# Optimization experiments

Hardware: AMD Instinct MI355X
Metric: run time of the kernel (lower is better)

The kernel has to match this reference:

```python
import jax, jax.numpy as jnp
import numpy as np

N, E, D = 100000, 200000, 300
NUM_EDGE_EMB = [6, 3]
BN_EPS = 1e-5


def setup_inputs() -> dict:
    key = jax.random.key(0)
    ks = jax.random.split(key, 10)
    return {
        "node_feats": jax.random.normal(ks[0], (N, D), jnp.float32),
        "src": jax.random.randint(ks[1], (E,), 0, N),
        "dst": jax.random.randint(ks[2], (E,), 0, N),
        "edge_feat0": jax.random.randint(ks[3], (E,), 0, NUM_EDGE_EMB[0]),
        "edge_feat1": jax.random.randint(ks[4], (E,), 0, NUM_EDGE_EMB[1]),
        # edge 'MLP' with num_layers=1 == Linear(num_emb, D) on one-hot indices
        "emb_w0": jax.random.normal(ks[5], (NUM_EDGE_EMB[0], D), jnp.float32) * 0.1,
        "emb_b0": jnp.zeros((D,), jnp.float32),
        "emb_w1": jax.random.normal(ks[6], (NUM_EDGE_EMB[1], D), jnp.float32) * 0.1,
        "emb_b1": jnp.zeros((D,), jnp.float32),
        # GIN update MLP: Linear(D, 2D) -> ReLU -> Linear(2D, D)
        "mlp_w1": jax.random.normal(ks[7], (D, 2 * D), jnp.float32) * (1.0 / np.sqrt(D)),
        "mlp_b1": jnp.zeros((2 * D,), jnp.float32),
        "mlp_w2": jax.random.normal(ks[8], (2 * D, D), jnp.float32) * (1.0 / np.sqrt(2 * D)),
        "mlp_b2": jnp.zeros((D,), jnp.float32),
        "bn_gamma": jnp.ones((D,), jnp.float32),
        "bn_beta": jnp.zeros((D,), jnp.float32),
    }


def reference(node_feats, src, dst, edge_feat0, edge_feat1,
              emb_w0, emb_b0, emb_w1, emb_b1,
              mlp_w1, mlp_b1, mlp_w2, mlp_b2,
              bn_gamma, bn_beta):
    n = node_feats.shape[0]
    # sum of per-variable edge embeddings (one-hot linear == lookup + bias)
    edge_emb = (emb_w0[edge_feat0] + emb_b0) + (emb_w1[edge_feat1] + emb_b1)  # (E, D)
    # u_add_e message, sum-reduce onto destination nodes
    msgs = node_feats[src] + edge_emb                                         # (E, D)
    agg = jax.ops.segment_sum(msgs, dst, num_segments=n)                      # (N, D)
    # GIN update MLP
    h = jax.nn.relu(agg @ mlp_w1 + mlp_b1)
    h = h @ mlp_w2 + mlp_b2
    # BatchNorm1d (training-mode forward: biased batch stats)
    mean = jnp.mean(h, axis=0)
    var = jnp.var(h, axis=0)
    h = (h - mean) * jax.lax.rsqrt(var + BN_EPS) * bn_gamma + bn_beta
    return h
```

## Files before the change

### kernel.cpp

```cpp
#include <hip/hip_runtime.h>
#include <stdint.h>


typedef __attribute__((ext_vector_type(8))) short short8;
typedef __attribute__((ext_vector_type(4))) short short4v;
typedef __attribute__((ext_vector_type(4))) float float4v;

__device__ inline unsigned short f2b(float f) {
  union { float f; unsigned int i; } v; v.f = f;
  unsigned int i = v.i;
  i += 0x7fffu + ((i >> 16) & 1u);
  return (unsigned short)(i >> 16);
}

__device__ __forceinline__ void gl_lds16(const short* g, short* l) {
  __builtin_amdgcn_global_load_lds(
      (const __attribute__((address_space(1))) unsigned int*)g,
      (__attribute__((address_space(3))) unsigned int*)l,
      16, 0, 0);
}

__global__ void transpose_pad(const float* __restrict__ in, short* __restrict__ out,
                              int R, int C, int outStride, int total) {
  int idx = blockIdx.x * blockDim.x + threadIdx.x;
  if (idx >= total) return;
  int r = idx / C, c = idx - r * C;
  out[(size_t)c * outStride + r] = (short)f2b(in[idx]);
}

__global__ void build_w01(const float* __restrict__ w0, const float* __restrict__ w1,
                          float* __restrict__ w01, int D, int NUM1, int total) {
  int i = blockIdx.x * blockDim.x + threadIdx.x;
  if (i >= total) return;
  int f01 = i / D, d = i - f01 * D;
  int f0 = f01 / NUM1, f1 = f01 - f0 * NUM1;
  w01[i] = w0[f0 * D + d] + w1[f1 * D + d];
}

__global__ void count_deg(const int* __restrict__ dst, int* __restrict__ deg, int E) {
  int e = blockIdx.x * blockDim.x + threadIdx.x;
  if (e < E) atomicAdd(&deg[dst[e]], 1);
}

__global__ void scan1(const int* __restrict__ deg, int* __restrict__ offp,
                      int* __restrict__ bsum, int n) {
  __shared__ int sh[256];
  const int t = threadIdx.x;
  const int base = blockIdx.x * 1024 + t * 4;
  int v[4], s = 0;
#pragma unroll
  for (int j = 0; j < 4; ++j) { int i = base + j; v[j] = (i < n) ? deg[i] : 0; s += v[j]; }
  sh[t] = s;
  __syncthreads();
  for (int d = 1; d < 256; d <<= 1) {
    int x = (t >= d) ? sh[t - d] : 0;
    __syncthreads();
    sh[t] += x;
    __syncthreads();
  }
  int excl = (t > 0) ? sh[t - 1] : 0;
  if (t == 255) bsum[blockIdx.x] = sh[255];
#pragma unroll
  for (int j = 0; j < 4; ++j) { int i = base + j; if (i < n) offp[i] = excl; excl += v[j]; }
}

__global__ void scan2(int* __restrict__ bsum, int nb) {
  __shared__ int sh[256];
  const int t = threadIdx.x;
  sh[t] = (t < nb) ? bsum[t] : 0;
  __syncthreads();
  for (int d = 1; d < 256; d <<= 1) {
    int x = (t >= d) ? sh[t - d] : 0;
    __syncthreads();
    sh[t] += x;
    __syncthreads();
  }
  if (t < nb) bsum[t] = (t > 0) ? sh[t - 1] : 0;
}

__global__ void fill_csr(const int* __restrict__ dst, const int* __restrict__ src,
                         const int* __restrict__ ef0, const int* __restrict__ ef1,
                         const int* __restrict__ offp, const int* __restrict__ bsum,
                         int* __restrict__ tmp, int2* __restrict__ ebp, int NUM1, int E) {
  int e = blockIdx.x * blockDim.x + threadIdx.x;
  if (e >= E) return;
  int dn = dst[e];
  int pos = offp[dn] + bsum[dn >> 10] + atomicAdd(&tmp[dn], 1);
  ebp[pos] = make_int2(src[e], ef0[e] * NUM1 + ef1[e]);
}

__global__ void gather_agg(const float* __restrict__ nf, const float* __restrict__ w01,
                           const float* __restrict__ b0f, const float* __restrict__ b1f,
                           const int* __restrict__ deg, const int* __restrict__ offp,
                           const int* __restrict__ bsum, const int2* __restrict__ ebp,
                           unsigned short* __restrict__ aggb,
                           int D, int ldab, int total) {
  int idx = blockIdx.x * blockDim.x + threadIdx.x;
  if (idx >= total) return;
  const int quads = ldab >> 2;
  int node = idx / quads;
  int q = idx - node * quads;
  int d = q * 4;
  unsigned short* op = &aggb[(size_t)node * ldab + d];
  if (d >= D) {
    short4v z = {0, 0, 0, 0};
    *(short4v*)op = z;
    return;
  }
  int dg = deg[node];
  int o = offp[node] + bsum[node >> 10];
  float4v acc = {0.f, 0.f, 0.f, 0.f};
  for (int j = 0; j < dg; ++j) {
    int2 p = ebp[o + j];
    float4v nv = *(const float4v*)&nf[(size_t)p.x * D + d];
    float4v wv = *(const float4v*)&w01[(size_t)p.y * D + d];
    acc += nv + wv;
  }
  float4v bb = *(const float4v*)&b0f[d];
  float4v b2v = *(const float4v*)&b1f[d];
  acc += (float)dg * (bb + b2v);
  short4v r;
#pragma unroll
  for (int j = 0; j < 4; ++j) r[j] = (short)f2b(acc[j]);
  *(short4v*)op = r;
}

template<bool RELU, bool STATS, bool CF32>
__global__ __launch_bounds__(256, 6)
void gemm_lds(const short* __restrict__ A, int lda,
              const short* __restrict__ BT, int ldbt,
              const float* __restrict__ bias,
              void* __restrict__ Cv, int ldc, int storeN,
              int M, int Nn, int KP, int ncolb,
              float* __restrict__ colsum, float* __restrict__ colsumsq) {
  constexpr int BM = 128, BN = 64, BK = 32;
  __shared__ __align__(16) short Al[BM * BK];
  __shared__ __align__(16) short Bl[BN * BK];

  const int nwg = gridDim.x;
  const int b = blockIdx.x;
  const int qq = nwg >> 3, rr = nwg & 7;
  const int xcd = b & 7, ii = b >> 3;
  const int w = ((xcd < rr) ? xcd * (qq + 1) : rr * (qq + 1) + (xcd - rr) * qq) + ii;
  const int by = w / ncolb, bx = w - by * ncolb;
  const int m0 = by * BM, n0 = bx * BN;

  const int t = threadIdx.x;
  const int wave = t >> 6, lane = t & 63, quad = lane >> 4, lr = lane & 15;
  const int wm = (wave >> 1) * 64, wn = (wave & 1) * 32;

  const int au = lane & 3;
  const int arow0 = (wave * 2 + 0) * 16 + (lane >> 2);
  const int arow1 = (wave * 2 + 1) * 16 + (lane >> 2);
  const int asw0 = au ^ ((arow0 ^ (arow0 >> 2)) & 3);
  const int asw1 = au ^ ((arow1 ^ (arow1 >> 2)) & 3);
  const short* asrc0 = A + (size_t)(m0 + arow0) * lda + asw0 * 8;
  const short* asrc1 = A + (size_t)(m0 + arow1) * lda + asw1 * 8;
  short* adst0 = &Al[(wave * 2 + 0) * 512];
  short* adst1 = &Al[(wave * 2 + 1) * 512];
  const int brow = wave * 16 + (lane >> 2);
  const int bsw = au ^ ((brow ^ (brow >> 2)) & 3);
  const short* bsrc = BT + (size_t)(n0 + brow) * ldbt + bsw * 8;
  short* bdst = &Bl[wave * 512];

  int aoff[4], boff[2];
#pragma unroll
  for (int mi = 0; mi < 4; ++mi) {
    int r = wm + mi * 16 + lr;
    aoff[mi] = r * BK + (quad ^ ((r ^ (r >> 2)) & 3)) * 8;
  }
#pragma unroll
  for (int ni = 0; ni < 2; ++ni) {
    int r = wn + ni * 16 + lr;
    boff[ni] = r * BK + (quad ^ ((r ^ (r >> 2)) & 3)) * 8;
  }

  const float4v fzero = {0.f, 0.f, 0.f, 0.f};
  float4v acc[4][2];
#pragma unroll
  for (int mi = 0; mi < 4; ++mi) {
    acc[mi][0] = fzero; acc[mi][1] = fzero;
  }

  for (int k0 = 0; k0 < KP; k0 += BK) {
    __syncthreads();
    gl_lds16(asrc0 + k0, adst0);
    gl_lds16(asrc1 + k0, adst1);
    gl_lds16(bsrc + k0, bdst);
    __syncthreads();
    short8 af[4], bfr[2];
#pragma unroll
    for (int mi = 0; mi < 4; ++mi) af[mi] = *(const short8*)&Al[aoff[mi]];
#pragma unroll
    for (int ni = 0; ni < 2; ++ni) bfr[ni] = *(const short8*)&Bl[boff[ni]];
#pragma unroll
    for (int mi = 0; mi < 4; ++mi) {
      acc[mi][0] = __builtin_amdgcn_mfma_f32_16x16x32_bf16(af[mi], bfr[0], acc[mi][0], 0, 0, 0);
      acc[mi][1] = __builtin_amdgcn_mfma_f32_16x16x32_bf16(af[mi], bfr[1], acc[mi][1], 0, 0, 0);
    }
  }

#pragma unroll
  for (int ni = 0; ni < 2; ++ni) {
    int gn = n0 + wn + ni * 16 + lr;
    bool store_c = (gn < storeN);
    bool ncol = (gn < Nn);
    float bv = ncol ? bias[gn] : 0.f;
    float s = 0.f, q = 0.f;
#pragma unroll
    for (int mi = 0; mi < 4; ++mi) {
      int gmb = m0 + wm + mi * 16 + quad * 4;
#pragma unroll
      for (int r = 0; r < 4; ++r) {
        int gm = gmb + r;
        float v = acc[mi][ni][r] + bv;
        if (RELU) v = fmaxf(v, 0.f);
        if (gm < M && store_c) {
          if constexpr (CF32) ((float*)Cv)[(size_t)gm * ldc + gn] = v;
          else ((unsigned short*)Cv)[(size_t)gm * ldc + gn] = f2b(v);
          if (STATS && ncol) { s += v; q += v * v; }
        }
      }
    }
    if constexpr (STATS) {
      s += __shfl_xor(s, 16); q += __shfl_xor(q, 16);
      s += __shfl_xor(s, 32); q += __shfl_xor(q, 32);
      if (quad == 0 && ncol) {
        unsafeAtomicAdd(&colsum[gn], s);
        unsafeAtomicAdd(&colsumsq[gn], q);
      }
    }
  }
}

__global__ void bn_finalize(const float* __restrict__ colsum, const float* __restrict__ colsumsq,
                            const float* __restrict__ gamma, const float* __restrict__ beta,
                            float2* __restrict__ ss, int D, float invN) {
  int d = blockIdx.x * blockDim.x + threadIdx.x;
  if (d >= D) return;
  float mean = colsum[d] * invN;
  float var = fmaxf(colsumsq[d] * invN - mean * mean, 0.f);
  float sc = rsqrtf(var + 1e-5f) * gamma[d];
  float sh = beta[d] - mean * sc;
  ss[d] = make_float2(sc, sh);
}

__global__ void bn_apply4(float4v* __restrict__ out, const float2* __restrict__ ss,
                          int total4, int cquads) {
  int idx = blockIdx.x * blockDim.x + threadIdx.x;
  if (idx >= total4) return;
  int c = (idx % cquads) * 4;
  float4v v = out[idx];
  float2 p0 = ss[c], p1 = ss[c + 1], p2 = ss[c + 2], p3 = ss[c + 3];
  v[0] = v[0] * p0.x + p0.y;
  v[1] = v[1] * p1.x + p1.y;
  v[2] = v[2] * p2.x + p2.y;
  v[3] = v[3] * p3.x + p3.y;
  out[idx] = v;
}

__global__ void bn_apply1(float* __restrict__ out, const float2* __restrict__ ss,
                          int total, int D) {
  int idx = blockIdx.x * blockDim.x + threadIdx.x;
  if (idx >= total) return;
  float2 p = ss[idx % D];
  out[idx] = out[idx] * p.x + p.y;
}

extern "C" void kernel_launch(void* const* d_in, const int* in_sizes, int n_in,
                              void* d_out, int out_size, void* d_ws, size_t ws_size,
                              hipStream_t stream) {
  const float* nf  = (const float*)d_in[0];
  const int*   src = (const int*)d_in[1];
  const int*   dst = (const int*)d_in[2];
  const int*   ef0 = (const int*)d_in[3];
  const int*   ef1 = (const int*)d_in[4];
  const float* ew0 = (const float*)d_in[5];
  const float* eb0 = (const float*)d_in[6];
  const float* ew1 = (const float*)d_in[7];
  const float* eb1 = (const float*)d_in[8];
  const float* w1  = (const float*)d_in[9];
  const float* b1  = (const float*)d_in[10];
  const float* w2  = (const float*)d_in[11];
  const float* b2  = (const float*)d_in[12];
  const float* gam = (const float*)d_in[13];
  const float* bet = (const float*)d_in[14];

  const int D = in_sizes[13];
  const int N = in_sizes[0] / D;
  const int E = in_sizes[1];
  const int H = in_sizes[10];
  const int NUM0 = in_sizes[5] / D;
  const int NUM1 = in_sizes[7] / D;
  const int KP1 = (D + 31) / 32 * 32;
  const int KP2 = (H + 31) / 32 * 32;
  const int NCB1 = (H + 63) / 64;
  const int NCB2 = (D + 63) / 64;
  const int BROWS1 = NCB1 * 64;
  const int BROWS2 = NCB2 * 64;
  const int nrowb = (N + 127) / 128;
  const int MP = nrowb * 128;
  const int nb  = (N + 1023) / 1024;

  char* ws = (char*)d_ws;
  size_t off = 0;
  float* colsum   = (float*)(ws + off); off += 4096;
  float* colsumsq = (float*)(ws + off); off += 4096;
  short* wT1      = (short*)(ws + off); off += (size_t)BROWS1 * KP1 * 2;
  short* wT2      = (short*)(ws + off); off += (size_t)BROWS2 * KP2 * 2;
  int*   deg      = (int*)(ws + off);   off += (size_t)N * 4;
  int*   tmp      = (int*)(ws + off);   off += (size_t)N * 4;
  size_t zero_bytes = off;
  float2* ss      = (float2*)(ws + off); off += 4096;
  float* w01      = (float*)(ws + off);  off += (size_t)NUM0 * NUM1 * D * 4;
  int*   offp     = (int*)(ws + off);    off += (size_t)N * 4;
  int*   bsum     = (int*)(ws + off);    off += 4096;
  int2*  ebp      = (int2*)(ws + off);   off += (size_t)E * 8;
  unsigned short* aggb = (unsigned short*)(ws + off); off += (size_t)MP * KP1 * 2;
  short* h1       = (short*)(ws + off);  off += (size_t)MP * KP2 * 2;

  hipMemsetAsync(d_ws, 0, zero_bytes, stream);

  {
    int tot = D * H;
    transpose_pad<<<(tot + 255) / 256, 256, 0, stream>>>(w1, wT1, D, H, KP1, tot);
  }
  {
    int tot = H * D;
    transpose_pad<<<(tot + 255) / 256, 256, 0, stream>>>(w2, wT2, H, D, KP2, tot);
  }
  {
    int tot = NUM0 * NUM1 * D;
    build_w01<<<(tot + 255) / 256, 256, 0, stream>>>(ew0, ew1, w01, D, NUM1, tot);
  }
  count_deg<<<(E + 255) / 256, 256, 0, stream>>>(dst, deg, E);
  scan1<<<nb, 256, 0, stream>>>(deg, offp, bsum, N);
  scan2<<<1, 256, 0, stream>>>(bsum, nb);
  fill_csr<<<(E + 255) / 256, 256, 0, stream>>>(dst, src, ef0, ef1, offp, bsum, tmp,
                                                ebp, NUM1, E);
  {
    int total = N * (KP1 / 4);
    gather_agg<<<(total + 255) / 256, 256, 0, stream>>>(
        nf, w01, eb0, eb1, deg, offp, bsum, ebp, aggb, D, KP1, total);
  }
  {
    gemm_lds<true, false, false><<<nrowb * NCB1, 256, 0, stream>>>(
        (const short*)aggb, KP1, wT1, KP1, b1,
        h1, KP2, KP2, N, H, KP1, NCB1, nullptr, nullptr);
  }
  {
    gemm_lds<false, true, true><<<nrowb * NCB2, 256, 0, stream>>>(
        h1, KP2, wT2, KP2, b2,
        d_out, D, D, N, D, KP2, NCB2, colsum, colsumsq);
  }
  bn_finalize<<<(D + 255) / 256, 256, 0, stream>>>(colsum, colsumsq, gam, bet, ss, D,
                                                   1.0f / (float)N);
  if ((D & 3) == 0) {
    int total4 = N * (D / 4);
    bn_apply4<<<(total4 + 255) / 256, 256, 0, stream>>>((float4v*)d_out, ss, total4, D / 4);
  } else {
    int tot = N * D;
    bn_apply1<<<(tot + 255) / 256, 256, 0, stream>>>((float*)d_out, ss, tot, D);
  }
}
```

Baseline: 583.2 us.

## Double-buffer LDS tiles in bf16 GEMM to overlap loads with MFMA

Splits the A and B shared-memory tiles into two buffers. The next K-slice is issued with global_load_lds into the alternate buffer while MFMAs consume the current one, and each iteration ends with a single barrier instead of two. The goal is to hide global-to-LDS latency behind matrix math. In exchange, LDS use per block doubles, which may limit how many blocks fit per CU at the requested launch bounds.

```diff
diff --git a/kernel.cpp b/kernel.cpp
--- a/kernel.cpp
+++ b/kernel.cpp
@@ -134,8 +134,8 @@
               int M, int Nn, int KP, int ncolb,
               float* __restrict__ colsum, float* __restrict__ colsumsq) {
   constexpr int BM = 128, BN = 64, BK = 32;
-  __shared__ __align__(16) short Al[BM * BK];
-  __shared__ __align__(16) short Bl[BN * BK];
+  __shared__ __align__(16) short Al[2][BM * BK];
+  __shared__ __align__(16) short Bl[2][BN * BK];
 
   const int nwg = gridDim.x;
   const int b = blockIdx.x;
@@ -156,12 +156,12 @@
   const int asw1 = au ^ ((arow1 ^ (arow1 >> 2)) & 3);
   const short* asrc0 = A + (size_t)(m0 + arow0) * lda + asw0 * 8;
   const short* asrc1 = A + (size_t)(m0 + arow1) * lda + asw1 * 8;
-  short* adst0 = &Al[(wave * 2 + 0) * 512];
-  short* adst1 = &Al[(wave * 2 + 1) * 512];
+  const int adst0 = (wave * 2 + 0) * 512;
+  const int adst1 = (wave * 2 + 1) * 512;
   const int brow = wave * 16 + (lane >> 2);
   const int bsw = au ^ ((brow ^ (brow >> 2)) & 3);
   const short* bsrc = BT + (size_t)(n0 + brow) * ldbt + bsw * 8;
-  short* bdst = &Bl[wave * 512];
+  const int bdst = wave * 512;
 
   int aoff[4], boff[2];
 #pragma unroll
@@ -182,22 +182,32 @@
     acc[mi][0] = fzero; acc[mi][1] = fzero;
   }
 
-  for (int k0 = 0; k0 < KP; k0 += BK) {
-    __syncthreads();
-    gl_lds16(asrc0 + k0, adst0);
-    gl_lds16(asrc1 + k0, adst1);
-    gl_lds16(bsrc + k0, bdst);
-    __syncthreads();
+  const int nk = KP / BK;
+  gl_lds16(asrc0, &Al[0][adst0]);
+  gl_lds16(asrc1, &Al[0][adst1]);
+  gl_lds16(bsrc, &Bl[0][bdst]);
+  __syncthreads();
+
+  int cur = 0;
+  for (int tk = 0; tk < nk; ++tk) {
+    if (tk + 1 < nk) {
+      int k0 = (tk + 1) * BK;
+      gl_lds16(asrc0 + k0, &Al[cur ^ 1][adst0]);
+      gl_lds16(asrc1 + k0, &Al[cur ^ 1][adst1]);
+      gl_lds16(bsrc + k0, &Bl[cur ^ 1][bdst]);
+    }
     short8 af[4], bfr[2];
 #pragma unroll
-    for (int mi = 0; mi < 4; ++mi) af[mi] = *(const short8*)&Al[aoff[mi]];
-#pragma unroll
-    for (int ni = 0; ni < 2; ++ni) bfr[ni] = *(const short8*)&Bl[boff[ni]];
+    for (int mi = 0; mi < 4; ++mi) af[mi] = *(const short8*)&Al[cur][aoff[mi]];
+#pragma unroll
+    for (int ni = 0; ni < 2; ++ni) bfr[ni] = *(const short8*)&Bl[cur][boff[ni]];
 #pragma unroll
     for (int mi = 0; mi < 4; ++mi) {
       acc[mi][0] = __builtin_amdgcn_mfma_f32_16x16x32_bf16(af[mi], bfr[0], acc[mi][0], 0, 0, 0);
       acc[mi][1] = __builtin_amdgcn_mfma_f32_16x16x32_bf16(af[mi], bfr[1], acc[mi][1], 0, 0, 0);
     }
+    __syncthreads();
+    cur ^= 1;
   }
 
 #pragma unroll
```

Result: slower. 602.0 us (+3.2%).

## Widen GEMM tile to 128x128 to double register reuse per wave

Applied to the files above, without the earlier changes.

Changes the MFMA GEMM block tile from 128x64 to 128x128. Each wave now computes a 64x64 sub-tile with a 4x4 accumulator grid, and the cooperative global-to-LDS loads and the padded weight column-block counts are adjusted to match. The aim is more MFMA work per LDS load and fewer A re-reads across column blocks. In exchange it uses more registers, lowers the occupancy hint from 6 to 3, and adds padding waste in N (H=600 pads to 640, D=300 pads to 384).

```diff
diff --git a/kernel.cpp b/kernel.cpp
--- a/kernel.cpp
+++ b/kernel.cpp
@@ -126,14 +126,14 @@
 }
 
 template<bool RELU, bool STATS, bool CF32>
-__global__ __launch_bounds__(256, 6)
+__global__ __launch_bounds__(256, 3)
 void gemm_lds(const short* __restrict__ A, int lda,
               const short* __restrict__ BT, int ldbt,
               const float* __restrict__ bias,
               void* __restrict__ Cv, int ldc, int storeN,
               int M, int Nn, int KP, int ncolb,
               float* __restrict__ colsum, float* __restrict__ colsumsq) {
-  constexpr int BM = 128, BN = 64, BK = 32;
+  constexpr int BM = 128, BN = 128, BK = 32;
   __shared__ __align__(16) short Al[BM * BK];
   __shared__ __align__(16) short Bl[BN * BK];
 
@@ -147,61 +147,65 @@
 
   const int t = threadIdx.x;
   const int wave = t >> 6, lane = t & 63, quad = lane >> 4, lr = lane & 15;
-  const int wm = (wave >> 1) * 64, wn = (wave & 1) * 32;
+  const int wm = (wave >> 1) * 64, wn = (wave & 1) * 64;
 
   const int au = lane & 3;
-  const int arow0 = (wave * 2 + 0) * 16 + (lane >> 2);
-  const int arow1 = (wave * 2 + 1) * 16 + (lane >> 2);
-  const int asw0 = au ^ ((arow0 ^ (arow0 >> 2)) & 3);
-  const int asw1 = au ^ ((arow1 ^ (arow1 >> 2)) & 3);
-  const short* asrc0 = A + (size_t)(m0 + arow0) * lda + asw0 * 8;
-  const short* asrc1 = A + (size_t)(m0 + arow1) * lda + asw1 * 8;
-  short* adst0 = &Al[(wave * 2 + 0) * 512];
-  short* adst1 = &Al[(wave * 2 + 1) * 512];
-  const int brow = wave * 16 + (lane >> 2);
-  const int bsw = au ^ ((brow ^ (brow >> 2)) & 3);
-  const short* bsrc = BT + (size_t)(n0 + brow) * ldbt + bsw * 8;
-  short* bdst = &Bl[wave * 512];
-
-  int aoff[4], boff[2];
+  int arow[2], brow[2];
+  const short* asrc[2];
+  const short* bsrc[2];
+  int adst[2], bdst[2];
+#pragma unroll
+  for (int l = 0; l < 2; ++l) {
+    int r = (l * 4 + wave) * 16 + (lane >> 2);
+    int sw = au ^ ((r ^ (r >> 2)) & 3);
+    arow[l] = r;
+    asrc[l] = A + (size_t)(m0 + r) * lda + sw * 8;
+    adst[l] = (l * 4 + wave) * 512;
+    brow[l] = r;
+    bsrc[l] = BT + (size_t)(n0 + r) * ldbt + sw * 8;
+    bdst[l] = (l * 4 + wave) * 512;
+  }
+
+  int aoff[4], boff[4];
 #pragma unroll
   for (int mi = 0; mi < 4; ++mi) {
     int r = wm + mi * 16 + lr;
     aoff[mi] = r * BK + (quad ^ ((r ^ (r >> 2)) & 3)) * 8;
   }
 #pragma unroll
-  for (int ni = 0; ni < 2; ++ni) {
+  for (int ni = 0; ni < 4; ++ni) {
     int r = wn + ni * 16 + lr;
     boff[ni] = r * BK + (quad ^ ((r ^ (r >> 2)) & 3)) * 8;
   }
 
   const float4v fzero = {0.f, 0.f, 0.f, 0.f};
-  float4v acc[4][2];
-#pragma unroll
-  for (int mi = 0; mi < 4; ++mi) {
-    acc[mi][0] = fzero; acc[mi][1] = fzero;
-  }
+  float4v acc[4][4];
+#pragma unroll
+  for (int mi = 0; mi < 4; ++mi)
+#pragma unroll
+    for (int ni = 0; ni < 4; ++ni) acc[mi][ni] = fzero;
 
   for (int k0 = 0; k0 < KP; k0 += BK) {
     __syncthreads();
-    gl_lds16(asrc0 + k0, adst0);
-    gl_lds16(asrc1 + k0, adst1);
-    gl_lds16(bsrc + k0, bdst);
-    __syncthreads();
-    short8 af[4], bfr[2];
+    gl_lds16(asrc[0] + k0, &Al[adst[0]]);
+    gl_lds16(asrc[1] + k0, &Al[adst[1]]);
+    gl_lds16(bsrc[0] + k0, &Bl[bdst[0]]);
+    gl_lds16(bsrc[1] + k0, &Bl[bdst[1]]);
+    __syncthreads();
+    short8 af[4], bfr[4];
 #pragma unroll
     for (int mi = 0; mi < 4; ++mi) af[mi] = *(const short8*)&Al[aoff[mi]];
 #pragma unroll
-    for (int ni = 0; ni < 2; ++ni) bfr[ni] = *(const short8*)&Bl[boff[ni]];
-#pragma unroll
-    for (int mi = 0; mi < 4; ++mi) {
-      acc[mi][0] = __builtin_amdgcn_mfma_f32_16x16x32_bf16(af[mi], bfr[0], acc[mi][0], 0, 0, 0);
-      acc[mi][1] = __builtin_amdgcn_mfma_f32_16x16x32_bf16(af[mi], bfr[1], acc[mi][1], 0, 0, 0);
-    }
-  }
-
-#pragma unroll
-  for (int ni = 0; ni < 2; ++ni) {
+    for (int ni = 0; ni < 4; ++ni) bfr[ni] = *(const short8*)&Bl[boff[ni]];
+#pragma unroll
+    for (int mi = 0; mi < 4; ++mi)
+#pragma unroll
+      for (int ni = 0; ni < 4; ++ni)
+        acc[mi][ni] = __builtin_amdgcn_mfma_f32_16x16x32_bf16(af[mi], bfr[ni], acc[mi][ni], 0, 0, 0);
+  }
+
+#pragma unroll
+  for (int ni = 0; ni < 4; ++ni) {
     int gn = n0 + wn + ni * 16 + lr;
     bool store_c = (gn < storeN);
     bool ncol = (gn < Nn);
@@ -294,10 +298,10 @@
   const int NUM1 = in_sizes[7] / D;
   const int KP1 = (D + 31) / 32 * 32;
   const int KP2 = (H + 31) / 32 * 32;
-  const int NCB1 = (H + 63) / 64;
-  const int NCB2 = (D + 63) / 64;
-  const int BROWS1 = NCB1 * 64;
-  const int BROWS2 = NCB2 * 64;
+  const int NCB1 = (H + 127) / 128;
+  const int NCB2 = (D + 127) / 128;
+  const int BROWS1 = NCB1 * 128;
+  const int BROWS2 = NCB2 * 128;
   const int nrowb = (N + 127) / 128;
   const int MP = nrowb * 128;
   const int nb  = (N + 1023) / 1024;
```

Result: slower. 624.0 us (+7.0%).
